# Optimization experiments

Hardware: AMD Instinct MI355X
Metric: run time of the kernel (lower is better)

## Reference

```python
import jax, jax.numpy as jnp
import numpy as np


def fps_single(xyz, npoint):
    """Furthest point sampling. xyz: [N,3] -> [npoint] int32 indices (first = 0)."""
    d0 = jnp.sum((xyz - xyz[0]) ** 2, axis=-1)  # [N]

    def body(dists, _):
        nxt = jnp.argmax(dists)
        d = jnp.sum((xyz - xyz[nxt]) ** 2, axis=-1)
        return jnp.minimum(dists, d), nxt.astype(jnp.int32)

    _, idxs = jax.lax.scan(body, d0, None, length=npoint - 1)
    return jnp.concatenate([jnp.zeros((1,), jnp.int32), idxs])


def setup_inputs() -> dict:
    key = jax.random.key(0)
    k1, k2 = jax.random.split(key)
    B, N, C = 4, 8192, 128
    points = jax.random.normal(k1, (B, N, 3), dtype=jnp.float32)
    features = jax.random.normal(k2, (B, C, N), dtype=jnp.float32)
    return {"points": points, "features": features, "npoint": 2048, "nsample": 16}


def reference(points, features, npoint, nsample):
    """FPS downsample -> kNN grouping (mean pool) -> three_nn inverse-distance interpolation.
    points: [B,N,3], features: [B,C,N]. Returns interpolated features [B,C,N]."""
    B, N, _ = points.shape
    # --- furthest point sampling (Sample module) ---
    fps_idx = jax.vmap(lambda p: fps_single(p, npoint))(points)          # [B,Q]
    xyz_q = jnp.take_along_axis(points, fps_idx[..., None], axis=1)      # [B,Q,3]
    # --- pairwise squared distances query->all (pdist2squared) ---
    sq = (jnp.sum(xyz_q ** 2, -1)[:, :, None]
          + jnp.sum(points ** 2, -1)[:, None, :]
          - 2.0 * jnp.einsum('bqd,bnd->bqn', xyz_q, points))             # [B,Q,N]
    sq = jnp.maximum(sq, 0.0)
    # --- kNN neighbors, drop self (SampleNeighbors, knn=True takes topk nsample+1 then [:,:,1:]) ---
    _, nbr = jax.lax.top_k(-sq, nsample + 1)                             # [B,Q,K+1]
    nbr = nbr[..., 1:]                                                   # [B,Q,K]
    grouped = jax.vmap(lambda f, idx: f[:, idx])(features, nbr)          # [B,C,Q,K]
    coarse = jnp.mean(grouped, axis=-1)                                  # [B,C,Q]
    # --- three_nn + inverse squared-distance interpolation (GraphFPModule) ---
    neg_d3, i3 = jax.lax.top_k(-jnp.swapaxes(sq, 1, 2), 3)               # [B,N,3]
    d3 = jnp.maximum(-neg_d3, 1e-10)                                     # squared dists, clamped
    inv = 1.0 / (d3 + 1e-8)
    w = inv / jnp.sum(inv, axis=-1, keepdims=True)                       # [B,N,3]
    f3 = jax.vmap(lambda f, idx: f[:, idx])(coarse, i3)                  # [B,C,N,3]
    out = jnp.sum(f3 * w[:, None, :, :], axis=-1)                        # [B,C,N]
    return out
```

## Files before the change

### kernel.cpp

```cpp
#include <hip/hip_runtime.h>
#include <cstdint>
#include <cstddef>

#define Bq   4
#define Nq   8192
#define Cq   128
#define NPq  2048
#define NSq  16
#define KSEL 17

__device__ __forceinline__ float rn_sq3(float x, float y, float z) {
  return __fadd_rn(__fadd_rn(__fmul_rn(x, x), __fmul_rn(y, y)), __fmul_rn(z, z));
}

__device__ __forceinline__ float sq_expand(float qx, float qy, float qz, float sq_,
                                           float px, float py, float pz, float sp_) {
  float dot = __fadd_rn(__fadd_rn(__fmul_rn(qx, px), __fmul_rn(qy, py)), __fmul_rn(qz, pz));
  float v = __fsub_rn(__fadd_rn(sq_, sp_), __fmul_rn(2.0f, dot));
  v = fmaxf(v, 0.0f);
  return __fadd_rn(v, 0.0f);
}

__global__ __launch_bounds__(256) void k_sump(const float* __restrict__ pts,
                                              float* __restrict__ sump) {
  int g = blockIdx.x * 256 + threadIdx.x;
  float x = pts[g * 3 + 0], y = pts[g * 3 + 1], z = pts[g * 3 + 2];
  sump[g] = rn_sq3(x, y, z);
}

__global__ __launch_bounds__(512) void k_fps(const float* __restrict__ pts,
                                             int* __restrict__ fps_idx) {
  const int b = blockIdx.x;
  const int tid = threadIdx.x;
  const int lane = tid & 63, wid = tid >> 6;
  const float* P = pts + (size_t)b * Nq * 3;

  __shared__ unsigned long long wkeys[8];
  __shared__ unsigned int bestp_sh;
  __shared__ float bx_sh, by_sh, bz_sh;

  float px[16], py[16], pz[16], dd[16];
#pragma unroll
  for (int k = 0; k < 16; k++) {
    int p = k * 512 + tid;
    px[k] = P[p * 3 + 0];
    py[k] = P[p * 3 + 1];
    pz[k] = P[p * 3 + 2];
  }
  float qx = P[0], qy = P[1], qz = P[2];
  unsigned long long lbest = 0ull;
#pragma unroll
  for (int k = 0; k < 16; k++) {
    int p = k * 512 + tid;
    float d = rn_sq3(__fsub_rn(px[k], qx), __fsub_rn(py[k], qy), __fsub_rn(pz[k], qz));
    dd[k] = d;
    unsigned long long key =
        ((unsigned long long)__float_as_uint(d) << 32) | (unsigned int)(~(unsigned int)p);
    lbest = key > lbest ? key : lbest;
  }
  if (tid == 0) fps_idx[b * NPq] = 0;

  for (int i = 1; i < NPq; i++) {
    unsigned long long key = lbest;
#pragma unroll
    for (int off = 32; off > 0; off >>= 1) {
      unsigned long long o = __shfl_down(key, off);
      key = o > key ? o : key;
    }
    if (lane == 0) wkeys[wid] = key;
    __syncthreads();
    if (tid == 0) {
      unsigned long long m = wkeys[0];
#pragma unroll
      for (int w = 1; w < 8; w++) m = wkeys[w] > m ? wkeys[w] : m;
      unsigned int p = ~(unsigned int)(m & 0xFFFFFFFFull);
      bestp_sh = p;
      fps_idx[b * NPq + i] = (int)p;
    }
    __syncthreads();
    unsigned int bp = bestp_sh;
    if ((bp & 511u) == (unsigned int)tid) {
      int k = bp >> 9;
      bx_sh = px[k]; by_sh = py[k]; bz_sh = pz[k];
    }
    __syncthreads();
    float cx = bx_sh, cy = by_sh, cz = bz_sh;
    lbest = 0ull;
#pragma unroll
    for (int k = 0; k < 16; k++) {
      float d = rn_sq3(__fsub_rn(px[k], cx), __fsub_rn(py[k], cy), __fsub_rn(pz[k], cz));
      float nd = fminf(dd[k], d);
      dd[k] = nd;
      int p = k * 512 + tid;
      unsigned long long kk =
          ((unsigned long long)__float_as_uint(nd) << 32) | (unsigned int)(~(unsigned int)p);
      lbest = kk > lbest ? kk : lbest;
    }
  }
}

__global__ __launch_bounds__(256) void k_gatherq(const float* __restrict__ pts,
                                                 const float* __restrict__ sump,
                                                 const int* __restrict__ fps_idx,
                                                 float* __restrict__ xyzq,
                                                 float* __restrict__ sumq) {
  int g = blockIdx.x * 256 + threadIdx.x;
  int b = g >> 11;
  int idx = fps_idx[g];
  int src = b * Nq + idx;
  xyzq[g * 3 + 0] = pts[src * 3 + 0];
  xyzq[g * 3 + 1] = pts[src * 3 + 1];
  xyzq[g * 3 + 2] = pts[src * 3 + 2];
  sumq[g] = sump[src];
}

__global__ __launch_bounds__(256) void k_knn_group(const float* __restrict__ pts,
                                                   const float* __restrict__ sump,
                                                   const float* __restrict__ xyzq,
                                                   const float* __restrict__ sumq,
                                                   const float* __restrict__ feats,
                                                   float* __restrict__ coarse_t) {
  const int blk = blockIdx.x;
  const int b = blk >> 11;
  const int tid = threadIdx.x;
  const int lane = tid & 63, wid = tid >> 6;
  const float* P = pts + (size_t)b * Nq * 3;
  const float* SP = sump + (size_t)b * Nq;

  __shared__ float sq_lds[Nq];
  __shared__ unsigned long long wkeys[4];
  __shared__ int sel[KSEL];

  float qx = xyzq[blk * 3 + 0], qy = xyzq[blk * 3 + 1], qz = xyzq[blk * 3 + 2];
  float sq_ = sumq[blk];

#pragma unroll
  for (int k = 0; k < 32; k++) {
    int p = k * 256 + tid;
    float x = P[p * 3 + 0], y = P[p * 3 + 1], z = P[p * 3 + 2];
    sq_lds[p] = sq_expand(qx, qy, qz, sq_, x, y, z, SP[p]);
  }
  __syncthreads();

  for (int r = 0; r < KSEL; r++) {
    unsigned long long best = ~0ull;
#pragma unroll
    for (int k = 0; k < 32; k++) {
      int p = k * 256 + tid;
      unsigned long long key =
          ((unsigned long long)__float_as_uint(sq_lds[p]) << 32) | (unsigned int)p;
      best = key < best ? key : best;
    }
#pragma unroll
    for (int off = 32; off > 0; off >>= 1) {
      unsigned long long o = __shfl_down(best, off);
      best = o < best ? o : best;
    }
    if (lane == 0) wkeys[wid] = best;
    __syncthreads();
    if (tid == 0) {
      unsigned long long m = wkeys[0];
      m = wkeys[1] < m ? wkeys[1] : m;
      m = wkeys[2] < m ? wkeys[2] : m;
      m = wkeys[3] < m ? wkeys[3] : m;
      int p = (int)(unsigned int)(m & 0xFFFFFFFFull);
      sel[r] = p;
      sq_lds[p] = __uint_as_float(0x7f800000u);
    }
    __syncthreads();
  }

  if (tid < Cq) {
    const float* F = feats + ((size_t)(b * Cq + tid)) * Nq;
    float acc = 0.0f;
#pragma unroll
    for (int j = 1; j < KSEL; j++) acc += F[sel[j]];
    coarse_t[(size_t)blk * Cq + tid] = acc * (1.0f / 16.0f);
  }
}

__device__ __forceinline__ void merge3(unsigned long long& a0, unsigned long long& a1,
                                       unsigned long long& a2, unsigned long long b0,
                                       unsigned long long b1, unsigned long long b2) {
  unsigned long long lo1 = a0 < b0 ? a0 : b0;
  unsigned long long hi1 = a0 < b0 ? b0 : a0;
  unsigned long long lo2 = a1 < b1 ? a1 : b1;
  unsigned long long hi2 = a1 < b1 ? b1 : a1;
  unsigned long long lo3 = a2 < b2 ? a2 : b2;
  unsigned long long c1 = hi1 < lo2 ? hi1 : lo2;
  unsigned long long m1 = hi1 < lo2 ? lo2 : hi1;
  unsigned long long m2 = hi2 < lo3 ? hi2 : lo3;
  a0 = lo1;
  a1 = c1;
  a2 = m1 < m2 ? m1 : m2;
}

__global__ __launch_bounds__(256) void k_three(const float* __restrict__ pts,
                                               const float* __restrict__ sump,
                                               const float* __restrict__ xyzq,
                                               const float* __restrict__ sumq,
                                               int* __restrict__ i0, int* __restrict__ i1,
                                               int* __restrict__ i2, float* __restrict__ w0,
                                               float* __restrict__ w1, float* __restrict__ w2) {
  const int wid = threadIdx.x >> 6, lane = threadIdx.x & 63;
  const int n = blockIdx.x * 4 + wid;
  const int b = n >> 13;
  float px = pts[n * 3 + 0], py = pts[n * 3 + 1], pz = pts[n * 3 + 2];
  float sp = sump[n];
  const float* XQ = xyzq + (size_t)b * NPq * 3;
  const float* SQ = sumq + (size_t)b * NPq;

  unsigned long long k0 = ~0ull, k1 = ~0ull, k2 = ~0ull;
#pragma unroll 4
  for (int j = 0; j < 32; j++) {
    int q = lane + j * 64;
    float v = sq_expand(XQ[q * 3 + 0], XQ[q * 3 + 1], XQ[q * 3 + 2], SQ[q], px, py, pz, sp);
    unsigned long long key = ((unsigned long long)__float_as_uint(v) << 32) | (unsigned int)q;
    if (key < k2) {
      if (key < k1) {
        k2 = k1;
        if (key < k0) { k1 = k0; k0 = key; } else { k1 = key; }
      } else {
        k2 = key;
      }
    }
  }
#pragma unroll
  for (int off = 32; off > 0; off >>= 1) {
    unsigned long long o0 = __shfl_down(k0, off);
    unsigned long long o1 = __shfl_down(k1, off);
    unsigned long long o2 = __shfl_down(k2, off);
    merge3(k0, k1, k2, o0, o1, o2);
  }
  if (lane == 0) {
    float v0 = __uint_as_float((unsigned int)(k0 >> 32));
    float v1 = __uint_as_float((unsigned int)(k1 >> 32));
    float v2 = __uint_as_float((unsigned int)(k2 >> 32));
    float d0 = fmaxf(v0, 1e-10f), d1 = fmaxf(v1, 1e-10f), d2 = fmaxf(v2, 1e-10f);
    float inv0 = 1.0f / (d0 + 1e-8f);
    float inv1 = 1.0f / (d1 + 1e-8f);
    float inv2 = 1.0f / (d2 + 1e-8f);
    float s = inv0 + inv1 + inv2;
    i0[n] = (int)(unsigned int)(k0 & 0xFFFFFFFFull);
    i1[n] = (int)(unsigned int)(k1 & 0xFFFFFFFFull);
    i2[n] = (int)(unsigned int)(k2 & 0xFFFFFFFFull);
    w0[n] = inv0 / s;
    w1[n] = inv1 / s;
    w2[n] = inv2 / s;
  }
}

__global__ __launch_bounds__(256) void k_interp(const float* __restrict__ coarse_t,
                                                const int* __restrict__ i0,
                                                const int* __restrict__ i1,
                                                const int* __restrict__ i2,
                                                const float* __restrict__ w0,
                                                const float* __restrict__ w1,
                                                const float* __restrict__ w2,
                                                float* __restrict__ out) {
  int g = blockIdx.x * 256 + threadIdx.x;
  int b = g >> 13, n = g & (Nq - 1);
  int a0 = i0[g], a1 = i1[g], a2 = i2[g];
  float u0 = w0[g], u1 = w1[g], u2 = w2[g];
  const float4* r0 = (const float4*)(coarse_t + ((size_t)b * NPq + a0) * Cq);
  const float4* r1 = (const float4*)(coarse_t + ((size_t)b * NPq + a1) * Cq);
  const float4* r2 = (const float4*)(coarse_t + ((size_t)b * NPq + a2) * Cq);
  float* O = out + (size_t)b * Cq * Nq + n;
#pragma unroll 4
  for (int cq = 0; cq < Cq / 4; cq++) {
    float4 f0 = r0[cq], f1 = r1[cq], f2 = r2[cq];
    float o0 = u0 * f0.x + u1 * f1.x + u2 * f2.x;
    float o1 = u0 * f0.y + u1 * f1.y + u2 * f2.y;
    float o2 = u0 * f0.z + u1 * f1.z + u2 * f2.z;
    float o3 = u0 * f0.w + u1 * f1.w + u2 * f2.w;
    O[(size_t)(cq * 4 + 0) * Nq] = o0;
    O[(size_t)(cq * 4 + 1) * Nq] = o1;
    O[(size_t)(cq * 4 + 2) * Nq] = o2;
    O[(size_t)(cq * 4 + 3) * Nq] = o3;
  }
}

extern "C" void kernel_launch(void* const* d_in, const int* in_sizes, int n_in,
                              void* d_out, int out_size, void* d_ws, size_t ws_size,
                              hipStream_t stream) {
  const float* pts = (const float*)d_in[0];
  const float* feats = (const float*)d_in[1];
  float* out = (float*)d_out;

  char* ws = (char*)d_ws;
  size_t off = 0;
  auto alloc = [&](size_t bytes) {
    void* p = ws + off;
    off += (bytes + 255) & ~(size_t)255;
    return p;
  };
  float* sump = (float*)alloc((size_t)Bq * Nq * 4);
  int* fps_idx = (int*)alloc((size_t)Bq * NPq * 4);
  float* xyzq = (float*)alloc((size_t)Bq * NPq * 3 * 4);
  float* sumq = (float*)alloc((size_t)Bq * NPq * 4);
  float* coarse_t = (float*)alloc((size_t)Bq * NPq * Cq * 4);
  int* i0 = (int*)alloc((size_t)Bq * Nq * 4);
  int* i1 = (int*)alloc((size_t)Bq * Nq * 4);
  int* i2 = (int*)alloc((size_t)Bq * Nq * 4);
  float* w0 = (float*)alloc((size_t)Bq * Nq * 4);
  float* w1 = (float*)alloc((size_t)Bq * Nq * 4);
  float* w2 = (float*)alloc((size_t)Bq * Nq * 4);

  k_sump<<<(Bq * Nq) / 256, 256, 0, stream>>>(pts, sump);
  k_fps<<<Bq, 512, 0, stream>>>(pts, fps_idx);
  k_gatherq<<<(Bq * NPq) / 256, 256, 0, stream>>>(pts, sump, fps_idx, xyzq, sumq);
  k_knn_group<<<Bq * NPq, 256, 0, stream>>>(pts, sump, xyzq, sumq, feats, coarse_t);
  k_three<<<(Bq * Nq) / 4, 256, 0, stream>>>(pts, sump, xyzq, sumq, i0, i1, i2, w0, w1, w2);
  k_interp<<<(Bq * Nq) / 256, 256, 0, stream>>>(coarse_t, i0, i1, i2, w0, w1, w2, out);
}
```

Measured before the change: 2.890 ms.

## Cut FPS iteration to one barrier with double-buffered keys and global centroid load

Each FPS iteration previously took three block barriers: one for the wave-key reduction, one for thread 0 to publish the winner, and one for the owning thread to publish its coordinates. Now every thread reduces the eight wave keys itself from a double-buffered shared array and reads the winning point's coordinates from global memory (likely cache-resident), so only one barrier per iteration remains. The per-thread argmax also tracks a float and a slot index instead of building 64-bit keys per element. The trade-off is a dependent global load on the serial critical path and redundant 8-way reductions in every thread.

```diff
diff --git a/kernel.cpp b/kernel.cpp
--- a/kernel.cpp
+++ b/kernel.cpp
@@ -35,9 +35,7 @@
   const int lane = tid & 63, wid = tid >> 6;
   const float* P = pts + (size_t)b * Nq * 3;
 
-  __shared__ unsigned long long wkeys[8];
-  __shared__ unsigned int bestp_sh;
-  __shared__ float bx_sh, by_sh, bz_sh;
+  __shared__ unsigned long long wkeys[2][8];
 
   float px[16], py[16], pz[16], dd[16];
 #pragma unroll
@@ -48,54 +46,50 @@
     pz[k] = P[p * 3 + 2];
   }
   float qx = P[0], qy = P[1], qz = P[2];
-  unsigned long long lbest = 0ull;
+  float bd = -1.0f;
+  int bk = 0;
 #pragma unroll
   for (int k = 0; k < 16; k++) {
-    int p = k * 512 + tid;
     float d = rn_sq3(__fsub_rn(px[k], qx), __fsub_rn(py[k], qy), __fsub_rn(pz[k], qz));
     dd[k] = d;
+    if (d > bd) { bd = d; bk = k; }
+  }
+  int bp = (bk << 9) + tid;
+  if (tid == 0) fps_idx[b * NPq] = 0;
+
+  for (int i = 1; i < NPq; i++) {
     unsigned long long key =
-        ((unsigned long long)__float_as_uint(d) << 32) | (unsigned int)(~(unsigned int)p);
-    lbest = key > lbest ? key : lbest;
-  }
-  if (tid == 0) fps_idx[b * NPq] = 0;
-
-  for (int i = 1; i < NPq; i++) {
-    unsigned long long key = lbest;
+        ((unsigned long long)__float_as_uint(bd) << 32) | (unsigned int)(~(unsigned int)bp);
 #pragma unroll
     for (int off = 32; off > 0; off >>= 1) {
       unsigned long long o = __shfl_down(key, off);
       key = o > key ? o : key;
     }
-    if (lane == 0) wkeys[wid] = key;
+    if (lane == 0) wkeys[i & 1][wid] = key;
     __syncthreads();
-    if (tid == 0) {
-      unsigned long long m = wkeys[0];
-#pragma unroll
-      for (int w = 1; w < 8; w++) m = wkeys[w] > m ? wkeys[w] : m;
-      unsigned int p = ~(unsigned int)(m & 0xFFFFFFFFull);
-      bestp_sh = p;
-      fps_idx[b * NPq + i] = (int)p;
-    }
-    __syncthreads();
-    unsigned int bp = bestp_sh;
-    if ((bp & 511u) == (unsigned int)tid) {
-      int k = bp >> 9;
-      bx_sh = px[k]; by_sh = py[k]; bz_sh = pz[k];
-    }
-    __syncthreads();
-    float cx = bx_sh, cy = by_sh, cz = bz_sh;
-    lbest = 0ull;
+
+    unsigned long long m = wkeys[i & 1][0];
+#pragma unroll
+    for (int w = 1; w < 8; w++) {
+      unsigned long long t = wkeys[i & 1][w];
+      m = t > m ? t : m;
+    }
+    unsigned int p = ~(unsigned int)m;
+    if (tid == 0) fps_idx[b * NPq + i] = (int)p;
+
+    const float* cp = P + 3u * p;
+    float cx = cp[0], cy = cp[1], cz = cp[2];
+
+    bd = -1.0f;
+    bk = 0;
 #pragma unroll
     for (int k = 0; k < 16; k++) {
       float d = rn_sq3(__fsub_rn(px[k], cx), __fsub_rn(py[k], cy), __fsub_rn(pz[k], cz));
       float nd = fminf(dd[k], d);
       dd[k] = nd;
-      int p = k * 512 + tid;
-      unsigned long long kk =
-          ((unsigned long long)__float_as_uint(nd) << 32) | (unsigned int)(~(unsigned int)p);
-      lbest = kk > lbest ? kk : lbest;
-    }
+      if (nd > bd) { bd = nd; bk = k; }
+    }
+    bp = (bk << 9) + tid;
   }
 }
 
```

New measurement: 2.770 ms. 4.1% less time.
